# Kernel optimization log

Hardware: AMD Instinct MI355X
Metric: run time of the kernel (lower is better)

Reference implementation:

```python
import jax, jax.numpy as jnp
import numpy as np


def _closest_distance_sum(p1, p2):
    # p1: [B, N, 3], p2: [B, M, 3]
    # squared Euclidean distance of each p1 point to nearest p2 point, summed.
    # d2[b,n,m] = |p1[b,n]|^2 + |p2[b,m]|^2 - 2 <p1[b,n], p2[b,m]>
    sq1 = jnp.sum(p1 * p1, axis=-1)                      # [B, N]
    sq2 = jnp.sum(p2 * p2, axis=-1)                      # [B, M]
    cross = jnp.einsum('bnd,bmd->bnm', p1, p2)           # [B, N, M]
    d2 = sq1[:, :, None] + sq2[:, None, :] - 2.0 * cross
    d2 = jnp.maximum(d2, 0.0)  # numerical floor (true sq-dist is >= 0)
    return jnp.sum(jnp.min(d2, axis=2))


def setup_inputs() -> dict:
    key = jax.random.key(0)
    k1, k2 = jax.random.split(key)
    shape_xyz = jax.random.normal(k1, (4, 8192, 3), dtype=jnp.float32)
    skel_xyz = jax.random.normal(k2, (4, 2048, 3), dtype=jnp.float32)
    return {"shape_xyz": shape_xyz, "skel_xyz": skel_xyz}


def reference(shape_xyz, skel_xyz):
    cd1 = _closest_distance_sum(shape_xyz, skel_xyz)
    cd2 = _closest_distance_sum(skel_xyz, shape_xyz)
    loss_cd = (cd1 + cd2) * 0.0001
    return loss_cd
```

## Files before the change

kernel.cpp:

```cpp
#include <hip/hip_runtime.h>


#define QPT    16
#define BIGF   3.4e38f

#define P2_OFF   1048576
#define PSUM_OFF 2097152
#define RBLOCKS  640

__device__ __forceinline__ float ror1(float v) {
    return __int_as_float(__builtin_amdgcn_update_dpp(
        0, __float_as_int(v), 0x13C, 0xF, 0xF, true));
}

__global__ __launch_bounds__(256) void chamfer_kernel(
    const float* __restrict__ shape,
    const float* __restrict__ skel,
    float* __restrict__ pw)
{
    const int b    = blockIdx.y;
    const int tid  = threadIdx.x;
    const int lane = tid & 63;

    const float* q; float* pbase; const float* ssrc;
    int q0, qstride;
    int x = blockIdx.x;
    if (x < 64) {
        const int qb = x >> 5, ch = x & 31;
        pbase   = pw + ((size_t)b * 32 + ch) * 8192;
        q0      = qb * 4096 + tid;
        qstride = 256;
        ssrc    = skel + ((size_t)b * 2048 + ch * 64) * 3;
        q       = shape + (size_t)b * 8192 * 3;
    } else {
        const int z = x - 64, half = tid >> 7;
        const int ch = 2 * z + half;
        pbase   = pw + P2_OFF + ((size_t)b * 128 + ch) * 2048;
        q0      = tid & 127;
        qstride = 128;
        ssrc    = shape + ((size_t)b * 8192 + z * 128 + half * 64) * 3;
        q       = skel + (size_t)b * 2048 * 3;
    }

    float tx = ssrc[lane * 3 + 0];
    float ty = ssrc[lane * 3 + 1];
    float tz = ssrc[lane * 3 + 2];
    float tw = fmaf(tx, tx, fmaf(ty, ty, tz * tz));

    const float* qp = q + (size_t)q0 * 3;
    const int qs3 = qstride * 3;
    float nqx[QPT], nqy[QPT], nqz[QPT], qsq[QPT], mn[QPT];
    #pragma unroll
    for (int k = 0; k < QPT; ++k) {
        float xq = qp[k * qs3 + 0];
        float yq = qp[k * qs3 + 1];
        float zq = qp[k * qs3 + 2];
        nqx[k] = -2.0f * xq; nqy[k] = -2.0f * yq; nqz[k] = -2.0f * zq;
        qsq[k] = xq * xq + yq * yq + zq * zq;
        mn[k]  = BIGF;
    }

    #pragma unroll 4
    for (int j = 0; j < 32; ++j) {
        float bx = ror1(tx), by = ror1(ty), bz = ror1(tz), bw = ror1(tw);
        #pragma unroll
        for (int k = 0; k < QPT; ++k) {
            float e0 = fmaf(nqx[k], tx,
                       fmaf(nqy[k], ty, fmaf(nqz[k], tz, tw)));
            float e1 = fmaf(nqx[k], bx,
                       fmaf(nqy[k], by, fmaf(nqz[k], bz, bw)));
            mn[k] = fminf(fminf(mn[k], e0), e1);
        }
        tx = ror1(bx); ty = ror1(by); tz = ror1(bz); tw = ror1(bw);
    }

    #pragma unroll
    for (int k = 0; k < QPT; ++k)
        pbase[q0 + k * qstride] = qsq[k] + mn[k];
}

__global__ __launch_bounds__(256) void reduce_kernel(
    const float* __restrict__ pw, float* __restrict__ psum)
{
    const int blk = blockIdx.x, tid = threadIdx.x;
    const int sub = tid & 3, qi = tid >> 2;

    float m = BIGF;
    if (blk < 512) {
        const int b  = blk >> 7;
        const int ql = ((blk & 127) << 6) + qi;
        const float* p = pw + (size_t)b * 32 * 8192 + ql;
        #pragma unroll
        for (int i = 0; i < 8; ++i)
            m = fminf(m, p[(sub * 8 + i) * 8192]);
    } else {
        const int z  = blk - 512;
        const int b  = z >> 5;
        const int ql = ((z & 31) << 6) + qi;
        const float* p = pw + P2_OFF + (size_t)b * 128 * 2048 + ql;
        #pragma unroll
        for (int i = 0; i < 32; ++i)
            m = fminf(m, p[(sub * 32 + i) * 2048]);
    }

    m = fminf(m, __shfl_xor(m, 1));
    m = fminf(m, __shfl_xor(m, 2));
    float s = (sub == 0) ? fmaxf(m, 0.0f) : 0.0f;

    #pragma unroll
    for (int off = 32; off > 0; off >>= 1)
        s += __shfl_down(s, off);

    __shared__ float wsum[4];
    const int lane = tid & 63, w = tid >> 6;
    if (lane == 0) wsum[w] = s;
    __syncthreads();
    if (tid == 0) psum[blk] = (wsum[0] + wsum[1]) + (wsum[2] + wsum[3]);
}

__global__ __launch_bounds__(256) void final_kernel(
    const float* __restrict__ psum, float* __restrict__ out)
{
    float s = psum[threadIdx.x] + psum[threadIdx.x + 256];
    if (threadIdx.x < 128) s += psum[threadIdx.x + 512];

    #pragma unroll
    for (int off = 32; off > 0; off >>= 1)
        s += __shfl_down(s, off);

    __shared__ float wsum[4];
    const int lane = threadIdx.x & 63, w = threadIdx.x >> 6;
    if (lane == 0) wsum[w] = s;
    __syncthreads();
    if (threadIdx.x == 0)
        out[0] = ((wsum[0] + wsum[1]) + (wsum[2] + wsum[3])) * 1.0e-4f;
}

extern "C" void kernel_launch(void* const* d_in, const int* in_sizes, int n_in,
                              void* d_out, int out_size, void* d_ws, size_t ws_size,
                              hipStream_t stream) {
    const float* shape = (const float*)d_in[0];
    const float* skel  = (const float*)d_in[1];
    float* out         = (float*)d_out;
    float* pw          = (float*)d_ws;

    chamfer_kernel<<<dim3(128, 4), 256, 0, stream>>>(shape, skel, pw);

    reduce_kernel<<<RBLOCKS, 256, 0, stream>>>(pw, pw + PSUM_OFF);
    final_kernel<<<1, 256, 0, stream>>>(pw + PSUM_OFF, out);
}
```

Measured before the change: 29.78 us.

## Broadcast target points from LDS and use packed FMA for pairs

```diff
diff --git a/kernel.cpp b/kernel.cpp
--- a/kernel.cpp
+++ b/kernel.cpp
@@ -4,32 +4,29 @@
 #define QPT    16
 #define BIGF   3.4e38f
 
+typedef float f32x2 __attribute__((ext_vector_type(2)));
+
 #define P2_OFF   1048576
 #define PSUM_OFF 2097152
 #define RBLOCKS  640
-
-__device__ __forceinline__ float ror1(float v) {
-    return __int_as_float(__builtin_amdgcn_update_dpp(
-        0, __float_as_int(v), 0x13C, 0xF, 0xF, true));
-}
 
 __global__ __launch_bounds__(256) void chamfer_kernel(
     const float* __restrict__ shape,
     const float* __restrict__ skel,
     float* __restrict__ pw)
 {
-    const int b    = blockIdx.y;
-    const int tid  = threadIdx.x;
-    const int lane = tid & 63;
+    const int b   = blockIdx.y;
+    const int tid = threadIdx.x;
 
     const float* q; float* pbase; const float* ssrc;
-    int q0, qstride;
+    int q0, qstride, lbase2, scount;
     int x = blockIdx.x;
     if (x < 64) {
         const int qb = x >> 5, ch = x & 31;
         pbase   = pw + ((size_t)b * 32 + ch) * 8192;
         q0      = qb * 4096 + tid;
         qstride = 256;
+        lbase2  = 0;  scount = 64;
         ssrc    = skel + ((size_t)b * 2048 + ch * 64) * 3;
         q       = shape + (size_t)b * 8192 * 3;
     } else {
@@ -38,40 +35,58 @@
         pbase   = pw + P2_OFF + ((size_t)b * 128 + ch) * 2048;
         q0      = tid & 127;
         qstride = 128;
-        ssrc    = shape + ((size_t)b * 8192 + z * 128 + half * 64) * 3;
+        lbase2  = half * 32;  scount = 128;
+        ssrc    = shape + ((size_t)b * 8192 + z * 128) * 3;
         q       = skel + (size_t)b * 2048 * 3;
     }
 
-    float tx = ssrc[lane * 3 + 0];
-    float ty = ssrc[lane * 3 + 1];
-    float tz = ssrc[lane * 3 + 2];
-    float tw = fmaf(tx, tx, fmaf(ty, ty, tz * tz));
+    __shared__ f32x2 lds2[256];
+
+    if (tid < scount) {
+        float tx = ssrc[tid * 3 + 0], ty = ssrc[tid * 3 + 1], tz = ssrc[tid * 3 + 2];
+        float tw = fmaf(tx, tx, fmaf(ty, ty, tz * tz));
+        const int pr = tid >> 1, c = tid & 1;
+        float* lf = (float*)lds2;
+        lf[(pr * 4 + 0) * 2 + c] = tx;
+        lf[(pr * 4 + 1) * 2 + c] = ty;
+        lf[(pr * 4 + 2) * 2 + c] = tz;
+        lf[(pr * 4 + 3) * 2 + c] = tw;
+    }
 
     const float* qp = q + (size_t)q0 * 3;
     const int qs3 = qstride * 3;
-    float nqx[QPT], nqy[QPT], nqz[QPT], qsq[QPT], mn[QPT];
+    f32x2 nqx[QPT], nqy[QPT], nqz[QPT];
+    float qsq[QPT], mn[QPT];
     #pragma unroll
     for (int k = 0; k < QPT; ++k) {
         float xq = qp[k * qs3 + 0];
         float yq = qp[k * qs3 + 1];
         float zq = qp[k * qs3 + 2];
-        nqx[k] = -2.0f * xq; nqy[k] = -2.0f * yq; nqz[k] = -2.0f * zq;
+        float nx = -2.0f * xq, ny = -2.0f * yq, nz = -2.0f * zq;
+        nqx[k][0] = nx; nqx[k][1] = nx;
+        nqy[k][0] = ny; nqy[k][1] = ny;
+        nqz[k][0] = nz; nqz[k][1] = nz;
         qsq[k] = xq * xq + yq * yq + zq * zq;
         mn[k]  = BIGF;
     }
 
+    __syncthreads();
+
     #pragma unroll 4
     for (int j = 0; j < 32; ++j) {
-        float bx = ror1(tx), by = ror1(ty), bz = ror1(tz), bw = ror1(tw);
+        const int p4 = (lbase2 + j) * 4;
+        f32x2 TX = lds2[p4 + 0];
+        f32x2 TY = lds2[p4 + 1];
+        f32x2 TZ = lds2[p4 + 2];
+        f32x2 TS = lds2[p4 + 3];
         #pragma unroll
         for (int k = 0; k < QPT; ++k) {
-            float e0 = fmaf(nqx[k], tx,
-                       fmaf(nqy[k], ty, fmaf(nqz[k], tz, tw)));
-            float e1 = fmaf(nqx[k], bx,
-                       fmaf(nqy[k], by, fmaf(nqz[k], bz, bw)));
-            mn[k] = fminf(fminf(mn[k], e0), e1);
+            f32x2 acc = TS;
+            asm("v_pk_fma_f32 %0, %1, %2, %0" : "+v"(acc) : "v"(nqz[k]), "v"(TZ));
+            asm("v_pk_fma_f32 %0, %1, %2, %0" : "+v"(acc) : "v"(nqy[k]), "v"(TY));
+            asm("v_pk_fma_f32 %0, %1, %2, %0" : "+v"(acc) : "v"(nqx[k]), "v"(TX));
+            mn[k] = fminf(fminf(mn[k], acc[0]), acc[1]);
         }
-        tx = ror1(bx); ty = ror1(by); tz = ror1(bz); tw = ror1(bw);
     }
 
     #pragma unroll
```

Measured after the change: 27.24 us. 1.09x faster.
